# Kernel tuning notes

Measured on AMD Instinct MI355X. Metric: run time of the kernel, lower is better.

## Reference

```python
import jax, jax.numpy as jnp
import numpy as np

B, S, C = 2, 2048, 1024          # batch, seq (= text_max_block_size), channels
H, D = 16, 64                    # num_heads, key_dim (C // H)
TEMP = 1e4                       # RoPE temperature
NEG_INF = -1e9


def rope(x):
    # x: [B, S, H, D]; interleaved-pair rotary embedding over sequence positions
    b, s, h, d = x.shape
    half = d // 2
    dim_t = TEMP ** (jnp.arange(half, dtype=jnp.float32) / half)      # [half]
    ang = jnp.arange(s, dtype=jnp.float32)[:, None] / dim_t            # [S, half]
    sin = jnp.sin(ang)[None, :, None, :]                               # [1,S,1,half]
    cos = jnp.cos(ang)[None, :, None, :]
    xr = x.reshape(b, s, h, half, 2)
    x1, x2 = xr[..., 0], xr[..., 1]
    out = jnp.stack([x1 * cos - x2 * sin, x2 * cos + x1 * sin], axis=-1)
    return out.reshape(b, s, h, d)


def setup_inputs() -> dict:
    key = jax.random.key(0)
    ks = jax.random.split(key, 5)
    w_scale = 0.02
    return {
        "x": jax.random.normal(ks[0], (B, S, C), jnp.float32),
        "w_qkv": jax.random.normal(ks[1], (C, 3 * C), jnp.float32) * w_scale,
        "q_bias": jax.random.normal(ks[2], (C,), jnp.float32) * w_scale,
        "v_bias": jax.random.normal(ks[3], (C,), jnp.float32) * w_scale,
        "w_out": jax.random.normal(ks[4], (C, C), jnp.float32) * w_scale,
    }


def reference(x, w_qkv, q_bias, v_bias, w_out):
    # fused QKV projection (no bias: qkv_bias=False)
    qkv = x @ w_qkv                                   # [B,S,3C]
    q, k, v = jnp.split(qkv, 3, axis=-1)
    # qv_bias=True: learnable bias on query and value only
    q = q + q_bias
    v = v + v_bias
    # inline RoPE on Q/K (PositionalEncodingFourierRot1D on [.., H, D/2, 2])
    q = rope(q.reshape(B, S, H, D))                   # [B,S,H,D]
    k = rope(k.reshape(B, S, H, D))
    v = v.reshape(B, S, H, D)
    scale = 1.0 / jnp.sqrt(jnp.float32(D))            # qk_scale <= 0 -> 1/sqrt(key_dim)
    scores = jnp.einsum("bqhd,bkhd->bhqk", q, k) * scale
    # CausalMask injected between scores and softmax
    causal = jnp.tril(jnp.ones((S, S), dtype=bool))
    scores = jnp.where(causal[None, None], scores, jnp.float32(NEG_INF))
    attn = jax.nn.softmax(scores, axis=-1)
    out = jnp.einsum("bhqk,bkhd->bqhd", attn, v).reshape(B, S, C)
    # output projection (return_weight=True, return_bias=False)
    return out @ w_out
```

## Files before the change

kernel.cpp:

```cpp
#include <hip/hip_runtime.h>
#include <stdint.h>

#define AS1 __attribute__((address_space(1)))
#define AS3 __attribute__((address_space(3)))

typedef __attribute__((ext_vector_type(8))) short bf16x8;
typedef __attribute__((ext_vector_type(4))) float f32x4;

__device__ __forceinline__ unsigned short f32_bf16(float f) {
  __bf16 b = (__bf16)f;
  union { __bf16 b; unsigned short u; } cv;
  cv.b = b;
  return cv.u;
}

__device__ __forceinline__ void async_ld16(const unsigned short* g, unsigned short* l) {
  __builtin_amdgcn_global_load_lds((const AS1 void*)g, (AS3 void*)l, 16, 0, 0);
}

__device__ __forceinline__ void transpose_tile(const float* __restrict__ src,
                                               unsigned short* __restrict__ dst,
                                               int K, int N, int nt, int kt,
                                               unsigned short (*tile)[65]) {
  int t = threadIdx.x;
  #pragma unroll
  for (int i = 0; i < 16; ++i) {
    int idx = t + i * 256;
    int r = idx >> 6, c = idx & 63;
    tile[r][c] = f32_bf16(src[(size_t)(kt * 64 + r) * N + nt * 64 + c]);
  }
  __syncthreads();
  #pragma unroll
  for (int i = 0; i < 16; ++i) {
    int idx = t + i * 256;
    int r = idx >> 6, c = idx & 63;
    dst[(size_t)(nt * 64 + r) * K + kt * 64 + c] = tile[c][r];
  }
}

__global__ __launch_bounds__(256) void prep(const float* __restrict__ x,
                                            const float* __restrict__ w_qkv,
                                            const float* __restrict__ w_out,
                                            unsigned short* __restrict__ Xb,
                                            unsigned short* __restrict__ WqkvT,
                                            unsigned short* __restrict__ WoT,
                                            float2* __restrict__ ropeT) {
  __shared__ unsigned short tile[64][65];
  int bid = blockIdx.x;
  if (bid < 4096) {
    int i = bid * 256 + threadIdx.x;
    float4 v = ((const float4*)x)[i];
    ushort4 o;
    o.x = f32_bf16(v.x); o.y = f32_bf16(v.y); o.z = f32_bf16(v.z); o.w = f32_bf16(v.w);
    ((ushort4*)Xb)[i] = o;
  } else if (bid < 4864) {
    int b2 = bid - 4096;
    transpose_tile(w_qkv, WqkvT, 1024, 3072, b2 % 48, b2 / 48, tile);
  } else if (bid < 5120) {
    int b2 = bid - 4864;
    transpose_tile(w_out, WoT, 1024, 1024, b2 % 16, b2 / 16, tile);
  } else {
    int idx = (bid - 5120) * 256 + threadIdx.x;
    int s = idx >> 5, p = idx & 31;
    float invf = exp2f((float)p * (-13.287712379549449f / 32.f));
    float sn, cs;
    __sincosf((float)s * invf, &sn, &cs);
    ropeT[idx] = make_float2(cs, sn);
  }
}

template <int KDIM>
__device__ __forceinline__ void gemm_core_k64(const unsigned short* __restrict__ A,
                                              const unsigned short* __restrict__ Bt,
                                              unsigned short* Als, unsigned short* Bls,
                                              int bm, int bn, f32x4 (&acc)[4][4]) {
  const int tid = threadIdx.x;
  const int w = tid >> 6, lane = tid & 63, quad = lane >> 4, l15 = lane & 15;
  const int wr = w >> 1, wc = w & 1;
  const int srow = lane >> 2, scol = (lane & 3) * 8;
  const unsigned short* Arow0 = A + (size_t)(bm * 128) * KDIM;
  const unsigned short* Brow0 = Bt + (size_t)(bn * 128) * KDIM;
  for (int k0 = 0; k0 < KDIM; k0 += 64) {
    __syncthreads();
    #pragma unroll
    for (int i = 0; i < 4; ++i) {
      int row = (i & 1) * 64 + w * 16 + srow;
      int kadd = (i >> 1) * 32 + scol;
      async_ld16(Arow0 + (size_t)row * KDIM + k0 + kadd, Als + i * 2048 + w * 512 + lane * 8);
      async_ld16(Brow0 + (size_t)row * KDIM + k0 + kadd, Bls + i * 2048 + w * 512 + lane * 8);
    }
    __syncthreads();
    #pragma unroll
    for (int kk2 = 0; kk2 < 2; ++kk2) {
      bf16x8 a[4], b[4];
      #pragma unroll
      for (int mi = 0; mi < 4; ++mi)
        a[mi] = *(const bf16x8*)(Als + kk2 * 4096 + (wr * 64 + mi * 16 + l15) * 32 + quad * 8);
      #pragma unroll
      for (int ni = 0; ni < 4; ++ni)
        b[ni] = *(const bf16x8*)(Bls + kk2 * 4096 + (wc * 64 + ni * 16 + l15) * 32 + quad * 8);
      #pragma unroll
      for (int mi = 0; mi < 4; ++mi)
        #pragma unroll
        for (int ni = 0; ni < 4; ++ni)
          acc[mi][ni] = __builtin_amdgcn_mfma_f32_16x16x32_bf16(a[mi], b[ni], acc[mi][ni], 0, 0, 0);
    }
  }
}

__global__ __launch_bounds__(256, 4) void qkv_gemm(const unsigned short* __restrict__ Xb,
                                                   const unsigned short* __restrict__ WqkvT,
                                                   const float* __restrict__ qbias,
                                                   const float* __restrict__ vbias,
                                                   const float2* __restrict__ ropeT,
                                                   unsigned short* __restrict__ Qg,
                                                   unsigned short* __restrict__ Kg,
                                                   unsigned short* __restrict__ Vtg) {
  __shared__ unsigned short shm[4 * 64 * 72];
  unsigned short* Als = shm;
  unsigned short* Bls = shm + 8192;
  f32x4 acc[4][4] = {};
  const int bn = blockIdx.x, bm = blockIdx.y;
  gemm_core_k64<1024>(Xb, WqkvT, Als, Bls, bm, bn, acc);
  __syncthreads();

  const int tid = threadIdx.x;
  const int w = tid >> 6, lane = tid & 63, quad = lane >> 4, l15 = lane & 15;
  const int wr = w >> 1, wc = w & 1;
  const int part = bn >> 3;
  const int cb = (bn & 7) * 128 + wc * 64;
  const int h = cb >> 6;
  const int m0 = bm * 128 + wr * 64;
  const int bb = m0 >> 11, s0 = m0 & 2047;
  unsigned short* Sw = shm + w * 4608;

  if (part < 2) {
    const float qscale = (part == 0) ? 0.18033688011112042f : 1.f;
    #pragma unroll
    for (int ni = 0; ni < 4; ++ni) {
      int dd = ni * 16 + l15;
      float bias = (part == 0) ? qbias[cb + dd] : 0.f;
      float sgn = (dd & 1) ? 1.f : -1.f;
      const float2* tp = ropeT + (size_t)s0 * 32 + (dd >> 1);
      #pragma unroll
      for (int mi = 0; mi < 4; ++mi) {
        #pragma unroll
        for (int r = 0; r < 4; ++r) {
          int sl = mi * 16 + quad * 4 + r;
          float val = acc[mi][ni][r] + bias;
          float partner = __shfl_xor(val, 1);
          float2 cssn = tp[sl * 32];
          val = (val * cssn.x + sgn * partner * cssn.y) * qscale;
          Sw[sl * 72 + dd] = f32_bf16(val);
        }
      }
    }
    unsigned short* dstp = (part == 0) ? Qg : Kg;
    const size_t base = ((size_t)(bb * 16 + h) * 2048 + s0) * 64;
    #pragma unroll
    for (int it = 0; it < 8; ++it) {
      int row = it * 8 + (lane >> 3), off = (lane & 7) * 8;
      bf16x8 v = *(const bf16x8*)(Sw + row * 72 + off);
      *(bf16x8*)(dstp + base + (size_t)row * 64 + off) = v;
    }
  } else {
    #pragma unroll
    for (int ni = 0; ni < 4; ++ni) {
      int dd = ni * 16 + l15;
      float bias = vbias[cb + dd];
      #pragma unroll
      for (int mi = 0; mi < 4; ++mi)
        #pragma unroll
        for (int r = 0; r < 4; ++r) {
          int sl = mi * 16 + quad * 4 + r;
          Sw[sl * 68 + dd] = f32_bf16(acc[mi][ni][r] + bias);
        }
    }
    const size_t vbase = (size_t)(bb * 16 + h) * 64 * 2048 + s0;
    #pragma unroll 4
    for (int dd = 0; dd < 64; ++dd) {
      unsigned short v = Sw[lane * 68 + dd];
      Vtg[vbase + (size_t)dd * 2048 + lane] = v;
    }
  }
}

__global__ __launch_bounds__(256, 4) void attn_fwd(const unsigned short* __restrict__ Qg,
                                                   const unsigned short* __restrict__ Kg,
                                                   const unsigned short* __restrict__ Vtg,
                                                   unsigned short* __restrict__ Og) {
  __shared__ unsigned short Kls[2][64 * 64];
  __shared__ unsigned short Vls[2][64 * 64];
  __shared__ unsigned short Pls[4][16 * 32];
  const int bid = blockIdx.x;
  const int ix = bid >> 3;
  const int bh = ((bid & 7) << 2) + (ix & 3);
  const int s = ix >> 2;
  const int m = s & 7, t = s >> 3;
  const int qt = (t == 0) ? m : (t == 1) ? (31 - m) : (t == 2) ? (8 + m) : (23 - m);
  const int h = bh & 15, b = bh >> 4;
  const int tid = threadIdx.x;
  const int w = tid >> 6, lane = tid & 63, quad = lane >> 4, l15 = lane & 15;
  const unsigned short* Qb = Qg + (size_t)bh * 2048 * 64;
  const unsigned short* Kb = Kg + (size_t)bh * 2048 * 64;
  const unsigned short* Vb = Vtg + (size_t)bh * 64 * 2048;
  const int q0 = qt * 64 + w * 16;

  bf16x8 aq[2];
  #pragma unroll
  for (int ki = 0; ki < 2; ++ki)
    aq[ki] = *(const bf16x8*)(Qb + (size_t)(q0 + l15) * 64 + ki * 32 + quad * 8);

  f32x4 o[4] = {};
  float l_st[4] = {0.f, 0.f, 0.f, 0.f};

  unsigned short* Pw = Pls[w];
  const int nkt = qt + 1;

  const int srow = tid >> 2, scol = (tid & 3) * 8;

  #pragma unroll
  for (int i = 0; i < 2; ++i) {
    async_ld16(Kb + (size_t)srow * 64 + i * 32 + scol, Kls[0] + i * 2048 + tid * 8);
    async_ld16(Vb + (size_t)srow * 2048 + i * 32 + scol, Vls[0] + i * 2048 + tid * 8);
  }

  for (int kt = 0; kt < nkt; ++kt) {
    __syncthreads();
    const int cur = kt & 1;
    if (kt + 1 < nkt) {
      const int nxt = cur ^ 1;
      #pragma unroll
      for (int i = 0; i < 2; ++i) {
        async_ld16(Kb + (size_t)((kt + 1) * 64 + srow) * 64 + i * 32 + scol,
                   Kls[nxt] + i * 2048 + tid * 8);
        async_ld16(Vb + (size_t)srow * 2048 + (kt + 1) * 64 + i * 32 + scol,
                   Vls[nxt] + i * 2048 + tid * 8);
      }
    }
    const unsigned short* Kbuf = Kls[cur];
    const unsigned short* Vbuf = Vls[cur];

    f32x4 sc[4] = {};
    #pragma unroll
    for (int ki = 0; ki < 2; ++ki) {
      bf16x8 bk[4];
      #pragma unroll
      for (int ni = 0; ni < 4; ++ni)
        bk[ni] = *(const bf16x8*)(Kbuf + ki * 2048 + (ni * 16 + l15) * 32 + quad * 8);
      #pragma unroll
      for (int ni = 0; ni < 4; ++ni)
        sc[ni] = __builtin_amdgcn_mfma_f32_16x16x32_bf16(aq[ki], bk[ni], sc[ni], 0, 0, 0);
    }

    if (kt == qt) {
      #pragma unroll
      for (int r = 0; r < 4; ++r) {
        int row = q0 + quad * 4 + r;
        #pragma unroll
        for (int ni = 0; ni < 4; ++ni) {
          bool masked = (kt * 64 + ni * 16 + l15) > row;
          float pv = __builtin_amdgcn_exp2f(sc[ni][r] - 8.f);
          pv = masked ? 0.f : pv;
          sc[ni][r] = pv;
          l_st[r] += pv;
        }
      }
    } else {
      #pragma unroll
      for (int r = 0; r < 4; ++r)
        #pragma unroll
        for (int ni = 0; ni < 4; ++ni) {
          float pv = __builtin_amdgcn_exp2f(sc[ni][r] - 8.f);
          sc[ni][r] = pv;
          l_st[r] += pv;
        }
    }

    #pragma unroll
    for (int k4 = 0; k4 < 2; ++k4) {
      #pragma unroll
      for (int nlh = 0; nlh < 2; ++nlh) {
        int nl = k4 * 2 + nlh;
        int ck = (nlh << 1) | (l15 >> 3);
        int cs = ck ^ quad;
        #pragma unroll
        for (int r = 0; r < 4; ++r) {
          int rw = quad * 4 + r;
          Pw[rw * 32 + cs * 8 + (l15 & 7)] = f32_bf16(sc[nl][r]);
        }
      }
      bf16x8 ap, bv[4];
      int csr = quad ^ ((l15 >> 2) & 3);
      ap = *(const bf16x8*)(Pw + l15 * 32 + csr * 8);
      #pragma unroll
      for (int di = 0; di < 4; ++di)
        bv[di] = *(const bf16x8*)(Vbuf + k4 * 2048 + (di * 16 + l15) * 32 + quad * 8);
      #pragma unroll
      for (int di = 0; di < 4; ++di)
        o[di] = __builtin_amdgcn_mfma_f32_16x16x32_bf16(ap, bv[di], o[di], 0, 0, 0);
    }
  }

  #pragma unroll
  for (int r = 0; r < 4; ++r) {
    float s2 = l_st[r];
    s2 += __shfl_xor(s2, 1);
    s2 += __shfl_xor(s2, 2);
    s2 += __shfl_xor(s2, 4);
    s2 += __shfl_xor(s2, 8);
    l_st[r] = 1.f / s2;
  }
  const size_t ob = ((size_t)(b * 2048 + q0)) * 1024 + h * 64;
  #pragma unroll
  for (int dh = 0; dh < 2; ++dh) {
    #pragma unroll
    for (int r = 0; r < 4; ++r) {
      float inv = l_st[r];
      int sl = quad * 4 + r;
      #pragma unroll
      for (int dl = 0; dl < 2; ++dl) {
        int di = dh * 2 + dl;
        int ck = dl * 2 + (l15 >> 3);
        int cs = ck ^ (sl & 3);
        Pw[sl * 32 + cs * 8 + (l15 & 7)] = f32_bf16(o[di][r] * inv);
      }
    }
    int row = lane >> 2;
    int cr = lane & 3;
    int crs = cr ^ (row & 3);
    bf16x8 v = *(const bf16x8*)(Pw + row * 32 + crs * 8);
    *(bf16x8*)(Og + ob + (size_t)row * 1024 + dh * 32 + cr * 8) = v;
  }
}

__global__ __launch_bounds__(256, 4) void out_gemm(const unsigned short* __restrict__ Og,
                                                   const unsigned short* __restrict__ WoT,
                                                   float* __restrict__ Cout) {
  __shared__ unsigned short Als[2 * 64 * 32];
  __shared__ unsigned short Bls[2 * 128 * 32];
  f32x4 acc[4][2] = {};
  const int bn = blockIdx.x, bm = blockIdx.y;
  const int tid = threadIdx.x;
  const int w = tid >> 6, lane = tid & 63, quad = lane >> 4, l15 = lane & 15;
  const int srow = lane >> 2, scol = (lane & 3) * 8;
  const unsigned short* Arow0 = Og + (size_t)(bm * 64) * 1024;
  const unsigned short* Brow0 = WoT + (size_t)(bn * 128) * 1024;
  for (int k0 = 0; k0 < 1024; k0 += 64) {
    __syncthreads();
    #pragma unroll
    for (int i = 0; i < 2; ++i) {
      int arow = w * 16 + srow;
      async_ld16(Arow0 + (size_t)arow * 1024 + k0 + i * 32 + scol,
                 Als + i * 2048 + w * 512 + lane * 8);
    }
    #pragma unroll
    for (int i = 0; i < 4; ++i) {
      int brow = (i & 1) * 64 + w * 16 + srow;
      int kadd = (i >> 1) * 32 + scol;
      async_ld16(Brow0 + (size_t)brow * 1024 + k0 + kadd,
                 Bls + i * 2048 + w * 512 + lane * 8);
    }
    __syncthreads();
    #pragma unroll
    for (int kk2 = 0; kk2 < 2; ++kk2) {
      bf16x8 a[4], b[2];
      #pragma unroll
      for (int mi = 0; mi < 4; ++mi)
        a[mi] = *(const bf16x8*)(Als + kk2 * 2048 + (mi * 16 + l15) * 32 + quad * 8);
      #pragma unroll
      for (int ni = 0; ni < 2; ++ni)
        b[ni] = *(const bf16x8*)(Bls + kk2 * 4096 + (w * 32 + ni * 16 + l15) * 32 + quad * 8);
      #pragma unroll
      for (int mi = 0; mi < 4; ++mi)
        #pragma unroll
        for (int ni = 0; ni < 2; ++ni)
          acc[mi][ni] = __builtin_amdgcn_mfma_f32_16x16x32_bf16(a[mi], b[ni], acc[mi][ni], 0, 0, 0);
    }
  }
  #pragma unroll
  for (int mi = 0; mi < 4; ++mi)
    #pragma unroll
    for (int r = 0; r < 4; ++r) {
      int mm = bm * 64 + mi * 16 + quad * 4 + r;
      #pragma unroll
      for (int ni = 0; ni < 2; ++ni) {
        int n = bn * 128 + w * 32 + ni * 16 + l15;
        Cout[(size_t)mm * 1024 + n] = acc[mi][ni][r];
      }
    }
}

extern "C" void kernel_launch(void* const* d_in, const int* in_sizes, int n_in,
                              void* d_out, int out_size, void* d_ws, size_t ws_size,
                              hipStream_t stream) {
  const float* x      = (const float*)d_in[0];
  const float* w_qkv  = (const float*)d_in[1];
  const float* q_bias = (const float*)d_in[2];
  const float* v_bias = (const float*)d_in[3];
  const float* w_out  = (const float*)d_in[4];
  float* out = (float*)d_out;

  char* ws = (char*)d_ws;
  unsigned short* Xb    = (unsigned short*)(ws);
  unsigned short* WqkvT = (unsigned short*)(ws + (8u  << 20));
  unsigned short* WoT   = (unsigned short*)(ws + (14u << 20));
  unsigned short* Qg    = (unsigned short*)(ws + (16u << 20));
  unsigned short* Kg    = (unsigned short*)(ws + (24u << 20));
  unsigned short* Vtg   = (unsigned short*)(ws + (32u << 20));
  unsigned short* Og    = (unsigned short*)(ws + (40u << 20));
  float2* ropeT         = (float2*)(ws + (48u << 20));

  prep<<<5376, 256, 0, stream>>>(x, w_qkv, w_out, Xb, WqkvT, WoT, ropeT);
  qkv_gemm<<<dim3(24, 32), 256, 0, stream>>>(Xb, WqkvT, q_bias, v_bias, ropeT, Qg, Kg, Vtg);
  attn_fwd<<<1024, 256, 0, stream>>>(Qg, Kg, Vtg, Og);
  out_gemm<<<dim3(8, 64), 256, 0, stream>>>(Og, WoT, out);
}
```

Before: 174.4 us.

## Double-buffer LDS tiles in QKV and output GEMM main loops

```diff
diff --git a/kernel.cpp b/kernel.cpp
--- a/kernel.cpp
+++ b/kernel.cpp
@@ -70,41 +70,50 @@
 }
 
 template <int KDIM>
-__device__ __forceinline__ void gemm_core_k64(const unsigned short* __restrict__ A,
-                                              const unsigned short* __restrict__ Bt,
-                                              unsigned short* Als, unsigned short* Bls,
-                                              int bm, int bn, f32x4 (&acc)[4][4]) {
+__device__ __forceinline__ void gemm_core_dbuf(const unsigned short* __restrict__ A,
+                                               const unsigned short* __restrict__ Bt,
+                                               unsigned short* Als, unsigned short* Bls,
+                                               int bm, int bn, f32x4 (&acc)[4][4]) {
   const int tid = threadIdx.x;
   const int w = tid >> 6, lane = tid & 63, quad = lane >> 4, l15 = lane & 15;
   const int wr = w >> 1, wc = w & 1;
   const int srow = lane >> 2, scol = (lane & 3) * 8;
   const unsigned short* Arow0 = A + (size_t)(bm * 128) * KDIM;
   const unsigned short* Brow0 = Bt + (size_t)(bn * 128) * KDIM;
-  for (int k0 = 0; k0 < KDIM; k0 += 64) {
+  #pragma unroll
+  for (int i = 0; i < 2; ++i) {
+    int row = i * 64 + w * 16 + srow;
+    async_ld16(Arow0 + (size_t)row * KDIM + scol, Als + i * 2048 + w * 512 + lane * 8);
+    async_ld16(Brow0 + (size_t)row * KDIM + scol, Bls + i * 2048 + w * 512 + lane * 8);
+  }
+  for (int k0 = 0; k0 < KDIM; k0 += 32) {
     __syncthreads();
-    #pragma unroll
-    for (int i = 0; i < 4; ++i) {
-      int row = (i & 1) * 64 + w * 16 + srow;
-      int kadd = (i >> 1) * 32 + scol;
-      async_ld16(Arow0 + (size_t)row * KDIM + k0 + kadd, Als + i * 2048 + w * 512 + lane * 8);
-      async_ld16(Brow0 + (size_t)row * KDIM + k0 + kadd, Bls + i * 2048 + w * 512 + lane * 8);
-    }
-    __syncthreads();
-    #pragma unroll
-    for (int kk2 = 0; kk2 < 2; ++kk2) {
-      bf16x8 a[4], b[4];
-      #pragma unroll
-      for (int mi = 0; mi < 4; ++mi)
-        a[mi] = *(const bf16x8*)(Als + kk2 * 4096 + (wr * 64 + mi * 16 + l15) * 32 + quad * 8);
+    const int cur = (k0 >> 5) & 1;
+    if (k0 + 32 < KDIM) {
+      const int nxt = cur ^ 1;
+      #pragma unroll
+      for (int i = 0; i < 2; ++i) {
+        int row = i * 64 + w * 16 + srow;
+        async_ld16(Arow0 + (size_t)row * KDIM + k0 + 32 + scol,
+                   Als + nxt * 4096 + i * 2048 + w * 512 + lane * 8);
+        async_ld16(Brow0 + (size_t)row * KDIM + k0 + 32 + scol,
+                   Bls + nxt * 4096 + i * 2048 + w * 512 + lane * 8);
+      }
+    }
+    const unsigned short* Ab = Als + cur * 4096;
+    const unsigned short* Bb = Bls + cur * 4096;
+    bf16x8 a[4], b[4];
+    #pragma unroll
+    for (int mi = 0; mi < 4; ++mi)
+      a[mi] = *(const bf16x8*)(Ab + (wr * 64 + mi * 16 + l15) * 32 + quad * 8);
+    #pragma unroll
+    for (int ni = 0; ni < 4; ++ni)
+      b[ni] = *(const bf16x8*)(Bb + (wc * 64 + ni * 16 + l15) * 32 + quad * 8);
+    #pragma unroll
+    for (int mi = 0; mi < 4; ++mi)
       #pragma unroll
       for (int ni = 0; ni < 4; ++ni)
-        b[ni] = *(const bf16x8*)(Bls + kk2 * 4096 + (wc * 64 + ni * 16 + l15) * 32 + quad * 8);
-      #pragma unroll
-      for (int mi = 0; mi < 4; ++mi)
-        #pragma unroll
-        for (int ni = 0; ni < 4; ++ni)
-          acc[mi][ni] = __builtin_amdgcn_mfma_f32_16x16x32_bf16(a[mi], b[ni], acc[mi][ni], 0, 0, 0);
-    }
+        acc[mi][ni] = __builtin_amdgcn_mfma_f32_16x16x32_bf16(a[mi], b[ni], acc[mi][ni], 0, 0, 0);
   }
 }
 
@@ -121,7 +130,7 @@
   unsigned short* Bls = shm + 8192;
   f32x4 acc[4][4] = {};
   const int bn = blockIdx.x, bm = blockIdx.y;
-  gemm_core_k64<1024>(Xb, WqkvT, Als, Bls, bm, bn, acc);
+  gemm_core_dbuf<1024>(Xb, WqkvT, Als, Bls, bm, bn, acc);
   __syncthreads();
 
   const int tid = threadIdx.x;
@@ -346,37 +355,44 @@
   const int srow = lane >> 2, scol = (lane & 3) * 8;
   const unsigned short* Arow0 = Og + (size_t)(bm * 64) * 1024;
   const unsigned short* Brow0 = WoT + (size_t)(bn * 128) * 1024;
-  for (int k0 = 0; k0 < 1024; k0 += 64) {
+  {
+    int arow = w * 16 + srow;
+    async_ld16(Arow0 + (size_t)arow * 1024 + scol, Als + w * 512 + lane * 8);
+    #pragma unroll
+    for (int i = 0; i < 2; ++i) {
+      int brow = i * 64 + w * 16 + srow;
+      async_ld16(Brow0 + (size_t)brow * 1024 + scol, Bls + i * 2048 + w * 512 + lane * 8);
+    }
+  }
+  for (int k0 = 0; k0 < 1024; k0 += 32) {
     __syncthreads();
-    #pragma unroll
-    for (int i = 0; i < 2; ++i) {
+    const int cur = (k0 >> 5) & 1;
+    if (k0 + 32 < 1024) {
+      const int nxt = cur ^ 1;
       int arow = w * 16 + srow;
-      async_ld16(Arow0 + (size_t)arow * 1024 + k0 + i * 32 + scol,
-                 Als + i * 2048 + w * 512 + lane * 8);
-    }
-    #pragma unroll
-    for (int i = 0; i < 4; ++i) {
-      int brow = (i & 1) * 64 + w * 16 + srow;
-      int kadd = (i >> 1) * 32 + scol;
-      async_ld16(Brow0 + (size_t)brow * 1024 + k0 + kadd,
-                 Bls + i * 2048 + w * 512 + lane * 8);
-    }
-    __syncthreads();
-    #pragma unroll
-    for (int kk2 = 0; kk2 < 2; ++kk2) {
-      bf16x8 a[4], b[2];
-      #pragma unroll
-      for (int mi = 0; mi < 4; ++mi)
-        a[mi] = *(const bf16x8*)(Als + kk2 * 2048 + (mi * 16 + l15) * 32 + quad * 8);
+      async_ld16(Arow0 + (size_t)arow * 1024 + k0 + 32 + scol,
+                 Als + nxt * 2048 + w * 512 + lane * 8);
+      #pragma unroll
+      for (int i = 0; i < 2; ++i) {
+        int brow = i * 64 + w * 16 + srow;
+        async_ld16(Brow0 + (size_t)brow * 1024 + k0 + 32 + scol,
+                   Bls + nxt * 4096 + i * 2048 + w * 512 + lane * 8);
+      }
+    }
+    const unsigned short* Ab = Als + cur * 2048;
+    const unsigned short* Bb = Bls + cur * 4096;
+    bf16x8 a[4], b[2];
+    #pragma unroll
+    for (int mi = 0; mi < 4; ++mi)
+      a[mi] = *(const bf16x8*)(Ab + (mi * 16 + l15) * 32 + quad * 8);
+    #pragma unroll
+    for (int ni = 0; ni < 2; ++ni)
+      b[ni] = *(const bf16x8*)(Bb + (w * 32 + ni * 16 + l15) * 32 + quad * 8);
+    #pragma unroll
+    for (int mi = 0; mi < 4; ++mi)
       #pragma unroll
       for (int ni = 0; ni < 2; ++ni)
-        b[ni] = *(const bf16x8*)(Bls + kk2 * 4096 + (w * 32 + ni * 16 + l15) * 32 + quad * 8);
-      #pragma unroll
-      for (int mi = 0; mi < 4; ++mi)
-        #pragma unroll
-        for (int ni = 0; ni < 2; ++ni)
-          acc[mi][ni] = __builtin_amdgcn_mfma_f32_16x16x32_bf16(a[mi], b[ni], acc[mi][ni], 0, 0, 0);
-    }
+        acc[mi][ni] = __builtin_amdgcn_mfma_f32_16x16x32_bf16(a[mi], b[ni], acc[mi][ni], 0, 0, 0);
   }
   #pragma unroll
   for (int mi = 0; mi < 4; ++mi)
```

New measurement: 179.9 us. 3.1% more time.
